# Performance work log

Measured on AMD Instinct MI355X. Metric: run time of the kernel, lower is better.

Reference implementation:

```python
import jax, jax.numpy as jnp
import numpy as np

B, N = 16, 2_000_000
NSIDE = 16
NPIX = 12 * NSIDE * NSIDE  # 3072
HID = 64
OUT = 100
LN_EPS = 1e-5


def _build_adj(npix, seed=0):
    # stand-in for healpix 8-neighbor adjacency: 8 neighbors per pixel, row-normalized
    rng = np.random.default_rng(seed)
    nbrs = rng.integers(0, npix, size=(npix, 8))
    adj = np.zeros((npix, npix), dtype=np.float32)
    rows = np.repeat(np.arange(npix), 8)
    adj[rows, nbrs.reshape(-1)] = 1.0
    deg = adj.sum(axis=1, keepdims=True)
    deg[deg == 0] = 1.0
    return jnp.asarray(adj / deg)


def _xavier(key, fan_in, fan_out):
    lim = float(np.sqrt(6.0 / (fan_in + fan_out)))
    return jax.random.uniform(key, (fan_in, fan_out), jnp.float32, -lim, lim)


def setup_inputs() -> dict:
    key = jax.random.key(0)
    ks = jax.random.split(key, 6)
    x = jax.random.normal(ks[0], (B, 3, N), jnp.float32)
    pix = jax.random.randint(ks[1], (B, N), 0, NPIX, jnp.int32)
    adj = _build_adj(NPIX)
    return {
        "x": x,
        "pix": pix,
        "adj": adj,
        "W1": _xavier(ks[2], 1, HID), "b1": jnp.zeros((HID,), jnp.float32),
        "g1": jnp.ones((HID,), jnp.float32), "be1": jnp.zeros((HID,), jnp.float32),
        "W2": _xavier(ks[3], HID, HID), "b2": jnp.zeros((HID,), jnp.float32),
        "g2": jnp.ones((HID,), jnp.float32), "be2": jnp.zeros((HID,), jnp.float32),
        "Wr": _xavier(ks[4], HID, OUT), "br": jnp.zeros((OUT,), jnp.float32),
        "scale": jnp.asarray(1.0, jnp.float32),
    }


def _graph_conv(h, adj, W, b, g, be):
    agg = jnp.einsum('pq,bqf->bpf', adj, h)
    o = agg @ W + b
    mu = o.mean(-1, keepdims=True)
    var = o.var(-1, keepdims=True)
    o = (o - mu) * jax.lax.rsqrt(var + LN_EPS) * g + be
    return jax.nn.relu(o)


def reference(x, pix, adj, W1, b1, g1, be1, W2, b2, g2, be2, Wr, br, scale):
    b_, _, n_ = x.shape
    npix = adj.shape[0]
    vals = x[:, 2, :]  # (B, N) -- F-2 == 1 channel; original broadcasts this scalar
    flat_idx = (jnp.arange(b_, dtype=pix.dtype)[:, None] * npix + pix).reshape(-1)
    pooled_sum = jax.ops.segment_sum(vals.reshape(-1), flat_idx, num_segments=b_ * npix).reshape(b_, npix)
    counts = jax.ops.segment_sum(jnp.ones((b_ * n_,), x.dtype), flat_idx, num_segments=b_ * npix).reshape(b_, npix)
    counts = jnp.where(counts == 0, jnp.asarray(1.0, x.dtype), counts)
    pooled = (pooled_sum / counts)[..., None]  # (B, npix, 1)
    h = _graph_conv(pooled, adj, W1, b1, g1, be1)
    h = _graph_conv(h, adj, W2, b2, g2, be2)
    out = h.mean(axis=1) @ Wr + br  # (B, OUT)
    return out * scale
```

## Files before the change

### kernel.cpp

```cpp
#include <hip/hip_runtime.h>

constexpr int BB   = 16;
constexpr int NN   = 2000000;
constexpr int NPIX = 3072;
constexpr int NOUT = 100;
constexpr int NB_POOL = 64;
constexpr float EPS = 1e-5f;

__device__ __forceinline__ float gatomic_add(float* p, float v) {
  return __hip_atomic_fetch_add(p, v, __ATOMIC_RELAXED, __HIP_MEMORY_SCOPE_AGENT);
}

__global__ __launch_bounds__(256) void k_pool(const float* __restrict__ x,
                                              const int* __restrict__ pix,
                                              unsigned long long* __restrict__ partial) {
  __shared__ unsigned long long hist[NPIX];
  const int b = blockIdx.y;
  for (int i = threadIdx.x; i < NPIX; i += 256) hist[i] = 0ull;
  __syncthreads();
  const float4* xv = (const float4*)(x + ((size_t)b * 3 + 2) * NN);
  const int4*   pv = (const int4*)(pix + (size_t)b * NN);
  const int nv = NN / 4;
  for (int i = blockIdx.x * 256 + threadIdx.x; i < nv; i += NB_POOL * 256) {
    float4 v = xv[i];
    int4   p = pv[i];
    unsigned long long e0 = (1ull << 44) + (unsigned long long)__float2uint_rn((v.x + 16.f) * 1048576.f);
    unsigned long long e1 = (1ull << 44) + (unsigned long long)__float2uint_rn((v.y + 16.f) * 1048576.f);
    unsigned long long e2 = (1ull << 44) + (unsigned long long)__float2uint_rn((v.z + 16.f) * 1048576.f);
    unsigned long long e3 = (1ull << 44) + (unsigned long long)__float2uint_rn((v.w + 16.f) * 1048576.f);
    atomicAdd(&hist[p.x], e0);
    atomicAdd(&hist[p.y], e1);
    atomicAdd(&hist[p.z], e2);
    atomicAdd(&hist[p.w], e3);
  }
  __syncthreads();
  unsigned long long* dst = partial + ((size_t)blockIdx.x * BB + b) * NPIX;
  for (int i = threadIdx.x; i < NPIX; i += 256) dst[i] = hist[i];
}

__global__ __launch_bounds__(256) void k_reduce(const unsigned long long* __restrict__ partial,
                                                float* __restrict__ gsum,
                                                float* __restrict__ gcnt,
                                                float* __restrict__ msum) {
  const int idx = blockIdx.x * 256 + threadIdx.x;
  if (idx < BB * 64) msum[idx] = 0.f;
  long long sf = 0, ct = 0;
  #pragma unroll 8
  for (int g = 0; g < NB_POOL; ++g) {
    unsigned long long p = partial[(size_t)g * (BB * NPIX) + idx];
    ct += (long long)(p >> 44);
    sf += (long long)(p & ((1ull << 44) - 1));
  }
  gcnt[idx] = (float)ct;
  gsum[idx] = (float)((double)sf * (1.0 / 1048576.0) - 16.0 * (double)ct);
}

__global__ __launch_bounds__(256) void k_extract(const float* __restrict__ adj,
                                                 int* __restrict__ cols,
                                                 float* __restrict__ vals,
                                                 int* __restrict__ rc) {
  const int p = blockIdx.x;
  __shared__ int cnt;
  if (threadIdx.x == 0) cnt = 0;
  __syncthreads();
  const float4* row = (const float4*)(adj + (size_t)p * NPIX);
  for (int i = threadIdx.x; i < NPIX / 4; i += 256) {
    float4 a = row[i];
    if (a.x != 0.f) { int s = atomicAdd(&cnt, 1); if (s < 8) { cols[p*8+s] = i*4+0; vals[p*8+s] = a.x; } }
    if (a.y != 0.f) { int s = atomicAdd(&cnt, 1); if (s < 8) { cols[p*8+s] = i*4+1; vals[p*8+s] = a.y; } }
    if (a.z != 0.f) { int s = atomicAdd(&cnt, 1); if (s < 8) { cols[p*8+s] = i*4+2; vals[p*8+s] = a.z; } }
    if (a.w != 0.f) { int s = atomicAdd(&cnt, 1); if (s < 8) { cols[p*8+s] = i*4+3; vals[p*8+s] = a.w; } }
  }
  __syncthreads();
  if (threadIdx.x == 0) rc[p] = min(cnt, 8);
}

__global__ __launch_bounds__(256) void k_conv1(const float* __restrict__ gsum,
                                               const float* __restrict__ gcnt,
                                               const int* __restrict__ cols,
                                               const float* __restrict__ vals,
                                               const int* __restrict__ rc,
                                               const float* __restrict__ W1,
                                               const float* __restrict__ b1,
                                               const float* __restrict__ g1,
                                               const float* __restrict__ be1,
                                               float* __restrict__ h1) {
  const int lane = threadIdx.x & 63;
  const int wid  = threadIdx.x >> 6;
  const int p = blockIdx.x * 4 + wid;
  const int b = blockIdx.y;
  const int n = rc[p];
  float contrib = 0.f;
  if (lane < n) {
    const int   q = cols[p*8 + lane];
    const float w = vals[p*8 + lane];
    const float s = gsum[b*NPIX + q];
    float c = gcnt[b*NPIX + q];
    c = (c == 0.f) ? 1.f : c;
    contrib = w * (s / c);
  }
  #pragma unroll
  for (int d = 1; d < 64; d <<= 1) contrib += __shfl_xor(contrib, d);
  const float agg = contrib;
  const float o = agg * W1[lane] + b1[lane];
  float ssum = o, ssq = o * o;
  #pragma unroll
  for (int d = 1; d < 64; d <<= 1) { ssum += __shfl_xor(ssum, d); ssq += __shfl_xor(ssq, d); }
  const float mu  = ssum * (1.f / 64.f);
  const float var = ssq * (1.f / 64.f) - mu * mu;
  float y = (o - mu) * rsqrtf(var + EPS) * g1[lane] + be1[lane];
  y = fmaxf(y, 0.f);
  h1[((size_t)b * NPIX + p) * 64 + lane] = y;
}

__global__ __launch_bounds__(256) void k_conv2(const float* __restrict__ h1,
                                               const int* __restrict__ cols,
                                               const float* __restrict__ vals,
                                               const int* __restrict__ rc,
                                               const float* __restrict__ W2,
                                               const float* __restrict__ b2,
                                               const float* __restrict__ g2,
                                               const float* __restrict__ be2,
                                               float* __restrict__ h2,
                                               float* __restrict__ msum) {
  __shared__ float Bs[64 * 64];
  __shared__ float Ast[64 * 68];
  __shared__ float colsum[64];
  const int b  = blockIdx.y;
  const int p0 = blockIdx.x * 64;
  const int tid = threadIdx.x;
  if (tid < 64) colsum[tid] = 0.f;
  for (int i = tid; i < 4096; i += 256) Bs[i] = W2[i];
  {
    const int r = tid >> 2;
    const int q = tid & 3;
    const int p = p0 + r;
    const int n = rc[p];
    float a[16];
    #pragma unroll
    for (int j = 0; j < 16; ++j) a[j] = 0.f;
    const float* hb = h1 + (size_t)b * NPIX * 64;
    for (int k = 0; k < n; ++k) {
      const int   qq = cols[p*8 + k];
      const float w  = vals[p*8 + k];
      const float4* src = (const float4*)(hb + (size_t)qq * 64 + q * 16);
      float4 s0 = src[0], s1 = src[1], s2 = src[2], s3 = src[3];
      a[0]  += w * s0.x; a[1]  += w * s0.y; a[2]  += w * s0.z; a[3]  += w * s0.w;
      a[4]  += w * s1.x; a[5]  += w * s1.y; a[6]  += w * s1.z; a[7]  += w * s1.w;
      a[8]  += w * s2.x; a[9]  += w * s2.y; a[10] += w * s2.z; a[11] += w * s2.w;
      a[12] += w * s3.x; a[13] += w * s3.y; a[14] += w * s3.z; a[15] += w * s3.w;
    }
    #pragma unroll
    for (int j = 0; j < 16; ++j) Ast[(q * 16 + j) * 68 + r] = a[j];
  }
  __syncthreads();
  const int lane = tid & 63;
  const int w    = tid >> 6;
  const int rt   = lane >> 4;
  const int ct   = lane & 15;
  const int r0   = w * 16 + rt * 4;
  const int c0   = ct * 4;
  float acc[4][4];
  #pragma unroll
  for (int i = 0; i < 4; ++i)
    #pragma unroll
    for (int j = 0; j < 4; ++j) acc[i][j] = 0.f;
  #pragma unroll 4
  for (int g = 0; g < 64; ++g) {
    const float4 av = *(const float4*)&Ast[g * 68 + r0];
    const float4 bv = *(const float4*)&Bs[g * 64 + c0];
    acc[0][0] += av.x * bv.x; acc[0][1] += av.x * bv.y; acc[0][2] += av.x * bv.z; acc[0][3] += av.x * bv.w;
    acc[1][0] += av.y * bv.x; acc[1][1] += av.y * bv.y; acc[1][2] += av.y * bv.z; acc[1][3] += av.y * bv.w;
    acc[2][0] += av.z * bv.x; acc[2][1] += av.z * bv.y; acc[2][2] += av.z * bv.z; acc[2][3] += av.z * bv.w;
    acc[3][0] += av.w * bv.x; acc[3][1] += av.w * bv.y; acc[3][2] += av.w * bv.z; acc[3][3] += av.w * bv.w;
  }
  const float4 b2v = *(const float4*)&b2[c0];
  const float4 g2v = *(const float4*)&g2[c0];
  const float4 bev = *(const float4*)&be2[c0];
  float* hb2 = h2 + ((size_t)b * NPIX + p0) * 64;
  float cs0 = 0.f, cs1 = 0.f, cs2 = 0.f, cs3 = 0.f;
  #pragma unroll
  for (int i = 0; i < 4; ++i) {
    float o0 = acc[i][0] + b2v.x, o1 = acc[i][1] + b2v.y;
    float o2 = acc[i][2] + b2v.z, o3 = acc[i][3] + b2v.w;
    float rs = o0 + o1 + o2 + o3;
    float rq = o0*o0 + o1*o1 + o2*o2 + o3*o3;
    #pragma unroll
    for (int d = 1; d < 16; d <<= 1) { rs += __shfl_xor(rs, d); rq += __shfl_xor(rq, d); }
    const float mu  = rs * (1.f / 64.f);
    const float var = rq * (1.f / 64.f) - mu * mu;
    const float inv = rsqrtf(var + EPS);
    float4 y;
    y.x = fmaxf((o0 - mu) * inv * g2v.x + bev.x, 0.f);
    y.y = fmaxf((o1 - mu) * inv * g2v.y + bev.y, 0.f);
    y.z = fmaxf((o2 - mu) * inv * g2v.z + bev.z, 0.f);
    y.w = fmaxf((o3 - mu) * inv * g2v.w + bev.w, 0.f);
    *(float4*)&hb2[(size_t)(r0 + i) * 64 + c0] = y;
    cs0 += y.x; cs1 += y.y; cs2 += y.z; cs3 += y.w;
  }
  atomicAdd(&colsum[c0+0], cs0);
  atomicAdd(&colsum[c0+1], cs1);
  atomicAdd(&colsum[c0+2], cs2);
  atomicAdd(&colsum[c0+3], cs3);
  __syncthreads();
  if (tid < 64) gatomic_add(&msum[b * 64 + tid], colsum[tid]);
}

__global__ __launch_bounds__(128) void k_head(const float* __restrict__ msum,
                                              const float* __restrict__ Wr,
                                              const float* __restrict__ br,
                                              const float* __restrict__ scale,
                                              float* __restrict__ out) {
  const int b = blockIdx.x;
  __shared__ float hm[64];
  if (threadIdx.x < 64) hm[threadIdx.x] = msum[b * 64 + threadIdx.x] * (1.f / NPIX);
  __syncthreads();
  const int o = threadIdx.x;
  if (o < NOUT) {
    float a = br[o];
    #pragma unroll 8
    for (int f = 0; f < 64; ++f) a += hm[f] * Wr[f * NOUT + o];
    out[b * NOUT + o] = a * scale[0];
  }
}

extern "C" void kernel_launch(void* const* d_in, const int* in_sizes, int n_in,
                              void* d_out, int out_size, void* d_ws, size_t ws_size,
                              hipStream_t stream) {
  const float* x    = (const float*)d_in[0];
  const int*   pix  = (const int*)d_in[1];
  const float* adj  = (const float*)d_in[2];
  const float* W1   = (const float*)d_in[3];
  const float* b1   = (const float*)d_in[4];
  const float* g1   = (const float*)d_in[5];
  const float* be1  = (const float*)d_in[6];
  const float* W2   = (const float*)d_in[7];
  const float* b2   = (const float*)d_in[8];
  const float* g2   = (const float*)d_in[9];
  const float* be2  = (const float*)d_in[10];
  const float* Wr   = (const float*)d_in[11];
  const float* br   = (const float*)d_in[12];
  const float* scale= (const float*)d_in[13];
  float* out = (float*)d_out;
  float* ws  = (float*)d_ws;

  unsigned long long* partial = (unsigned long long*)ws;
  float* gsum = ws + 6291456;
  float* gcnt = ws + 6340608;
  float* msum = ws + 6389760;
  int*   cols = (int*)(ws + 6390784);
  float* vals = ws + 6415360;
  int*   rc   = (int*)(ws + 6439936);
  float* h1   = ws + 6443008;
  float* h2   = h1 + 3145728;

  k_pool   <<<dim3(NB_POOL, BB), 256, 0, stream>>>(x, pix, partial);
  k_reduce <<<BB * NPIX / 256,   256, 0, stream>>>(partial, gsum, gcnt, msum);
  k_extract<<<NPIX,              256, 0, stream>>>(adj, cols, vals, rc);
  k_conv1  <<<dim3(NPIX/4, BB),  256, 0, stream>>>(gsum, gcnt, cols, vals, rc,
                                                   W1, b1, g1, be1, h1);
  k_conv2  <<<dim3(NPIX/64, BB), 256, 0, stream>>>(h1, cols, vals, rc,
                                                   W2, b2, g2, be2, h2, msum);
  k_head   <<<BB,                128, 0, stream>>>(msum, Wr, br, scale, out);
}
```

Baseline: 616.8 us.

## Replace shared-memory pooling histograms with direct global 64-bit atomics

Pooling now adds each packed (count,sum) value straight into one global bin array per batch with device-scope 64-bit atomics. This removes the per-block shared histograms, the partial-buffer writeback and the separate reduce kernel, and conv1 decodes the packed bins itself. Grid width doubles and a memset zeroes the bins and msum. The cost is 32M global atomics spread over 49K bins, which may contend far more than LDS atomics did.

```diff
diff --git a/kernel.cpp b/kernel.cpp
--- a/kernel.cpp
+++ b/kernel.cpp
@@ -4,55 +4,36 @@
 constexpr int NN   = 2000000;
 constexpr int NPIX = 3072;
 constexpr int NOUT = 100;
-constexpr int NB_POOL = 64;
+constexpr int NBX_POOL = 128;
 constexpr float EPS = 1e-5f;
 
 __device__ __forceinline__ float gatomic_add(float* p, float v) {
   return __hip_atomic_fetch_add(p, v, __ATOMIC_RELAXED, __HIP_MEMORY_SCOPE_AGENT);
 }
+__device__ __forceinline__ void gatomic_add_u64(unsigned long long* p, unsigned long long v) {
+  __hip_atomic_fetch_add(p, v, __ATOMIC_RELAXED, __HIP_MEMORY_SCOPE_AGENT);
+}
 
 __global__ __launch_bounds__(256) void k_pool(const float* __restrict__ x,
                                               const int* __restrict__ pix,
-                                              unsigned long long* __restrict__ partial) {
-  __shared__ unsigned long long hist[NPIX];
+                                              unsigned long long* __restrict__ gbins) {
   const int b = blockIdx.y;
-  for (int i = threadIdx.x; i < NPIX; i += 256) hist[i] = 0ull;
-  __syncthreads();
   const float4* xv = (const float4*)(x + ((size_t)b * 3 + 2) * NN);
   const int4*   pv = (const int4*)(pix + (size_t)b * NN);
+  unsigned long long* bb = gbins + (size_t)b * NPIX;
   const int nv = NN / 4;
-  for (int i = blockIdx.x * 256 + threadIdx.x; i < nv; i += NB_POOL * 256) {
+  for (int i = blockIdx.x * 256 + threadIdx.x; i < nv; i += NBX_POOL * 256) {
     float4 v = xv[i];
     int4   p = pv[i];
     unsigned long long e0 = (1ull << 44) + (unsigned long long)__float2uint_rn((v.x + 16.f) * 1048576.f);
     unsigned long long e1 = (1ull << 44) + (unsigned long long)__float2uint_rn((v.y + 16.f) * 1048576.f);
     unsigned long long e2 = (1ull << 44) + (unsigned long long)__float2uint_rn((v.z + 16.f) * 1048576.f);
     unsigned long long e3 = (1ull << 44) + (unsigned long long)__float2uint_rn((v.w + 16.f) * 1048576.f);
-    atomicAdd(&hist[p.x], e0);
-    atomicAdd(&hist[p.y], e1);
-    atomicAdd(&hist[p.z], e2);
-    atomicAdd(&hist[p.w], e3);
-  }
-  __syncthreads();
-  unsigned long long* dst = partial + ((size_t)blockIdx.x * BB + b) * NPIX;
-  for (int i = threadIdx.x; i < NPIX; i += 256) dst[i] = hist[i];
-}
-
-__global__ __launch_bounds__(256) void k_reduce(const unsigned long long* __restrict__ partial,
-                                                float* __restrict__ gsum,
-                                                float* __restrict__ gcnt,
-                                                float* __restrict__ msum) {
-  const int idx = blockIdx.x * 256 + threadIdx.x;
-  if (idx < BB * 64) msum[idx] = 0.f;
-  long long sf = 0, ct = 0;
-  #pragma unroll 8
-  for (int g = 0; g < NB_POOL; ++g) {
-    unsigned long long p = partial[(size_t)g * (BB * NPIX) + idx];
-    ct += (long long)(p >> 44);
-    sf += (long long)(p & ((1ull << 44) - 1));
-  }
-  gcnt[idx] = (float)ct;
-  gsum[idx] = (float)((double)sf * (1.0 / 1048576.0) - 16.0 * (double)ct);
+    gatomic_add_u64(&bb[p.x], e0);
+    gatomic_add_u64(&bb[p.y], e1);
+    gatomic_add_u64(&bb[p.z], e2);
+    gatomic_add_u64(&bb[p.w], e3);
+  }
 }
 
 __global__ __launch_bounds__(256) void k_extract(const float* __restrict__ adj,
@@ -75,8 +56,7 @@
   if (threadIdx.x == 0) rc[p] = min(cnt, 8);
 }
 
-__global__ __launch_bounds__(256) void k_conv1(const float* __restrict__ gsum,
-                                               const float* __restrict__ gcnt,
+__global__ __launch_bounds__(256) void k_conv1(const unsigned long long* __restrict__ gbins,
                                                const int* __restrict__ cols,
                                                const float* __restrict__ vals,
                                                const int* __restrict__ rc,
@@ -94,10 +74,12 @@
   if (lane < n) {
     const int   q = cols[p*8 + lane];
     const float w = vals[p*8 + lane];
-    const float s = gsum[b*NPIX + q];
-    float c = gcnt[b*NPIX + q];
-    c = (c == 0.f) ? 1.f : c;
-    contrib = w * (s / c);
+    const unsigned long long pb = gbins[(size_t)b * NPIX + q];
+    const float ct = (float)(unsigned int)(pb >> 44);
+    const double sf = (double)(pb & ((1ull << 44) - 1));
+    const float c = (ct == 0.f) ? 1.f : ct;
+    const float mean = (float)(sf * (1.0 / 1048576.0) - 16.0 * (double)ct) / c;
+    contrib = w * mean;
   }
   #pragma unroll
   for (int d = 1; d < 64; d <<= 1) contrib += __shfl_xor(contrib, d);
@@ -244,22 +226,21 @@
   float* out = (float*)d_out;
   float* ws  = (float*)d_ws;
 
-  unsigned long long* partial = (unsigned long long*)ws;
-  float* gsum = ws + 6291456;
-  float* gcnt = ws + 6340608;
-  float* msum = ws + 6389760;
-  int*   cols = (int*)(ws + 6390784);
-  float* vals = ws + 6415360;
-  int*   rc   = (int*)(ws + 6439936);
-  float* h1   = ws + 6443008;
+  unsigned long long* gbins = (unsigned long long*)ws;
+  float* msum = ws + 98304;
+  int*   cols = (int*)(ws + 99328);
+  float* vals = ws + 123904;
+  int*   rc   = (int*)(ws + 148480);
+  float* h1   = ws + 151552;
   float* h2   = h1 + 3145728;
 
-  k_pool   <<<dim3(NB_POOL, BB), 256, 0, stream>>>(x, pix, partial);
-  k_reduce <<<BB * NPIX / 256,   256, 0, stream>>>(partial, gsum, gcnt, msum);
-  k_extract<<<NPIX,              256, 0, stream>>>(adj, cols, vals, rc);
-  k_conv1  <<<dim3(NPIX/4, BB),  256, 0, stream>>>(gsum, gcnt, cols, vals, rc,
-                                                   W1, b1, g1, be1, h1);
-  k_conv2  <<<dim3(NPIX/64, BB), 256, 0, stream>>>(h1, cols, vals, rc,
-                                                   W2, b2, g2, be2, h2, msum);
-  k_head   <<<BB,                128, 0, stream>>>(msum, Wr, br, scale, out);
-}
+  hipMemsetAsync(ws, 0, (size_t)(98304 + 1024) * sizeof(float), stream);
+
+  k_pool   <<<dim3(NBX_POOL, BB), 256, 0, stream>>>(x, pix, gbins);
+  k_extract<<<NPIX,               256, 0, stream>>>(adj, cols, vals, rc);
+  k_conv1  <<<dim3(NPIX/4, BB),   256, 0, stream>>>(gbins, cols, vals, rc,
+                                                    W1, b1, g1, be1, h1);
+  k_conv2  <<<dim3(NPIX/64, BB),  256, 0, stream>>>(h1, cols, vals, rc,
+                                                    W2, b2, g2, be2, h2, msum);
+  k_head   <<<BB,                 128, 0, stream>>>(msum, Wr, br, scale, out);
+}
```

Measured after the change: 1.853 ms. 200% more time.
